# Optimization experiments

Hardware: AMD Instinct MI355X
Metric: run time of the kernel (lower is better)

The kernel has to match this reference:

```python
import jax, jax.numpy as jnp
import numpy as np

N_NODES = 50000
N_EDGES = 1000000
H_DIM = 128
OUT_DIM = 64
N_RELS = 16  # num_bases == num_rels


def setup_inputs() -> dict:
    key = jax.random.key(0)
    ks = jax.random.split(key, 12)
    node_ids = jnp.arange(N_NODES, dtype=jnp.int64) if jax.config.jax_enable_x64 else jnp.arange(N_NODES, dtype=jnp.int32)
    src = jax.random.randint(ks[0], (N_EDGES,), 0, N_NODES)
    dst = jax.random.randint(ks[1], (N_EDGES,), 0, N_NODES)
    etype = jax.random.randint(ks[2], (N_EDGES,), 0, N_RELS)
    norm = jax.random.uniform(ks[3], (N_EDGES, 1), dtype=jnp.float32)
    s1 = 1.0 / np.sqrt(H_DIM)
    s2 = 1.0 / np.sqrt(OUT_DIM)
    emb = jax.random.normal(ks[4], (N_NODES, H_DIM), dtype=jnp.float32)
    V1 = jax.random.normal(ks[5], (N_RELS, H_DIM, H_DIM), dtype=jnp.float32) * s1
    comp1 = jax.random.normal(ks[6], (N_RELS, N_RELS), dtype=jnp.float32) * (1.0 / np.sqrt(N_RELS))
    bias1 = jnp.zeros((H_DIM,), dtype=jnp.float32)
    V2 = jax.random.normal(ks[7], (N_RELS, H_DIM, OUT_DIM), dtype=jnp.float32) * s2
    comp2 = jax.random.normal(ks[8], (N_RELS, N_RELS), dtype=jnp.float32) * (1.0 / np.sqrt(N_RELS))
    bias2 = jnp.zeros((OUT_DIM,), dtype=jnp.float32)
    return {"node_ids": node_ids, "src": src, "dst": dst, "etype": etype, "norm": norm,
            "emb": emb, "V1": V1, "comp1": comp1, "bias1": bias1,
            "V2": V2, "comp2": comp2, "bias2": bias2}


def _rel_graph_conv(x, src, dst, etype, norm, V, comp, bias, num_nodes):
    # Basis decomposition: W_r = sum_b comp[r, b] * V_b  -> [R, in, out]
    W = jnp.einsum('rb,bio->rio', comp, V)
    # Per-relation transform of all nodes: [R, N, out]
    Y = jnp.einsum('ni,rio->rno', x, W)
    # Per-edge message: gather (etype, src) then scale by norm  -> [E, out]
    m = Y[etype, src] * norm
    # Scatter-add to destination nodes
    h = jax.ops.segment_sum(m, dst, num_segments=num_nodes)
    return h + bias


def reference(node_ids, src, dst, etype, norm, emb, V1, comp1, bias1, V2, comp2, bias2):
    x = emb[node_ids]  # [N, H]
    h = jax.nn.relu(_rel_graph_conv(x, src, dst, etype, norm, V1, comp1, bias1, x.shape[0]))
    h = _rel_graph_conv(h, src, dst, etype, norm, V2, comp2, bias2, x.shape[0])
    return h
```

## Files before the change

### kernel.cpp

```cpp
#include <hip/hip_runtime.h>


typedef short bf16x8 __attribute__((ext_vector_type(8)));
typedef float f32x4 __attribute__((ext_vector_type(4)));

#define RELS 16
#define HDIM 128
#define DSTBLK 66
#define MT_P 5
#define CHUNK 32
#define MAXBINS 12288

__device__ inline unsigned short f2bf(float f) {
  unsigned int u = __float_as_uint(f);
  unsigned int r = u + 0x7FFFu + ((u >> 16) & 1u);
  return (unsigned short)(r >> 16);
}

__global__ void cvt_bf16(const float* __restrict__ in, unsigned short* __restrict__ out, int n8) {
  int i = blockIdx.x * blockDim.x + threadIdx.x;
  if (i >= n8) return;
  float4 a = ((const float4*)in)[i * 2];
  float4 b = ((const float4*)in)[i * 2 + 1];
  uint4 o;
  o.x = (unsigned)f2bf(a.x) | ((unsigned)f2bf(a.y) << 16);
  o.y = (unsigned)f2bf(a.z) | ((unsigned)f2bf(a.w) << 16);
  o.z = (unsigned)f2bf(b.x) | ((unsigned)f2bf(b.y) << 16);
  o.w = (unsigned)f2bf(b.z) | ((unsigned)f2bf(b.w) << 16);
  ((uint4*)out)[i] = o;
}

__global__ void compute_w(const float* __restrict__ comp, const float* __restrict__ V,
                          unsigned short* __restrict__ Wt, int IO) {
  int idx = blockIdx.x * blockDim.x + threadIdx.x;
  if (idx >= RELS * IO * HDIM) return;
  int k = idx & (HDIM - 1);
  int o = (idx >> 7) % IO;
  int r = idx / (IO * HDIM);
  float s = 0.f;
#pragma unroll
  for (int b = 0; b < RELS; b++)
    s = fmaf(comp[r * RELS + b], V[(size_t)b * HDIM * IO + (size_t)k * IO + o], s);
  Wt[idx] = f2bf(s);
}

__global__ void hist_bins(const int* __restrict__ dst, const int* __restrict__ etype,
                          int n, int nbins, int* __restrict__ counts) {
  __shared__ int lh[MAXBINS];
  for (int j = threadIdx.x; j < nbins; j += blockDim.x) lh[j] = 0;
  __syncthreads();
  for (int i = blockIdx.x * blockDim.x + threadIdx.x; i < n; i += gridDim.x * blockDim.x)
    atomicAdd(&lh[(dst[i] / DSTBLK) * RELS + etype[i]], 1);
  __syncthreads();
  for (int j = threadIdx.x; j < nbins; j += blockDim.x) {
    int c = lh[j];
    if (c) atomicAdd(&counts[j], c);
  }
}

__global__ void scan_offsets(const int* __restrict__ counts, int* __restrict__ offsets, int nbins) {
  __shared__ int csum[256];
  const int t = threadIdx.x;
  const int CH = (nbins + 255) / 256;
  int lo = t * CH, hi = min(lo + CH, nbins);
  int s = 0;
  for (int i = lo; i < hi; i++) s += (counts[i] + 15) & ~15;
  csum[t] = s;
  __syncthreads();
#pragma unroll
  for (int d = 1; d < 256; d <<= 1) {
    int v = (t >= d) ? csum[t - d] : 0;
    __syncthreads();
    csum[t] += v;
    __syncthreads();
  }
  int run = (t == 0) ? 0 : csum[t - 1];
  for (int i = lo; i < hi; i++) {
    offsets[i] = run;
    run += (counts[i] + 15) & ~15;
  }
  if (lo < nbins && hi == nbins) offsets[nbins] = run;
}

__global__ void scatter_bins(const int* __restrict__ src, const int* __restrict__ dst,
                             const int* __restrict__ etype, const float* __restrict__ norm,
                             int n, const int* __restrict__ offsets, int* __restrict__ cursor,
                             uint2* __restrict__ ebuf) {
  for (int i = blockIdx.x * blockDim.x + threadIdx.x; i < n; i += gridDim.x * blockDim.x) {
    int d = dst[i];
    int blk = d / DSTBLK;
    int b = blk * RELS + etype[i];
    int p = offsets[b] + atomicAdd(&cursor[b], 1);
    ebuf[p] = make_uint2((unsigned)src[i] | ((unsigned)(d - blk * DSTBLK) << 20),
                         __float_as_uint(norm[i]));
  }
}

template <int OUT, bool BF16_RELU_OUT>
__launch_bounds__(256, 3)
__global__ void rgcn_layer(const unsigned short* __restrict__ Xb,
                           const unsigned short* __restrict__ Wt,
                           const uint2* __restrict__ ebuf,
                           const int* __restrict__ offsets, const int* __restrict__ counts,
                           const float* __restrict__ bias, void* __restrict__ Hout,
                           int nNodes) {
  constexpr int NT = OUT / 64;
  __shared__ __align__(16) unsigned short xs[2][CHUNK][136];
  __shared__ __align__(16) unsigned short ys[OUT][40];
  __shared__ __align__(16) unsigned short pmat[2][80][40];

  const int t = threadIdx.x;
  const int w = t >> 6;
  const int lane = t & 63;
  const int quad = lane >> 4;
  const int l16 = lane & 15;
  const int r0 = t >> 4;
  const int k8 = t & 15;
  const bool isHandler = (t & 7) == 0;
  const int myCol = t >> 3;
  const int nodeBase = blockIdx.x * DSTBLK;
  const int binBase = blockIdx.x * RELS;
  const int colBase = w * (OUT / 4);

  for (int i = t; i < 2 * CHUNK * 136 / 8; i += 256) ((uint4*)xs)[i] = make_uint4(0, 0, 0, 0);
  for (int i = t; i < OUT * 40 / 8; i += 256) ((uint4*)ys)[i] = make_uint4(0, 0, 0, 0);
  for (int i = t; i < 2 * 80 * 40 / 8; i += 256) ((uint4*)pmat)[i] = make_uint4(0, 0, 0, 0);

  f32x4 pacc[MT_P][NT] = {};

  int bin = 0, base = 0, binEnd = 0, realEnd = 0;
  for (; bin < RELS; bin++) {
    base = offsets[binBase + bin];
    binEnd = offsets[binBase + bin + 1];
    if (base < binEnd) { realEnd = base + counts[binBase + bin]; break; }
  }

  __syncthreads();

  int pdA = -1, pdB = -1;
  if (bin < RELS) {
    int nR = min(CHUNK, realEnd - base);
    if (r0 < nR) {
      uint2 e = ebuf[base + r0];
      *(uint4*)&xs[0][r0][k8 * 8] = *(const uint4*)(Xb + (size_t)(e.x & 0xFFFFFu) * HDIM + k8 * 8);
    }
    if (16 + r0 < nR) {
      uint2 e = ebuf[base + 16 + r0];
      *(uint4*)&xs[0][16 + r0][k8 * 8] = *(const uint4*)(Xb + (size_t)(e.x & 0xFFFFFu) * HDIM + k8 * 8);
    }
    if (isHandler && myCol < nR) {
      uint2 m = ebuf[base + myCol];
      int dl = (int)(m.x >> 20) & 127;
      pmat[0][dl][myCol] = f2bf(__uint_as_float(m.y));
      pdB = dl;
    }
  }
  __syncthreads();

  int cb = 0;
  int curRel = -1;
  bf16x8 wf[4][NT];

  while (bin < RELS) {
    const int nRows = min(CHUNK, realEnd - base);

    if (bin != curRel) {
      curRel = bin;
      const unsigned short* Wr = Wt + (size_t)bin * OUT * HDIM;
#pragma unroll
      for (int ks = 0; ks < 4; ks++)
#pragma unroll
        for (int nt = 0; nt < NT; nt++)
          wf[ks][nt] = *(const bf16x8*)(Wr + (size_t)(colBase + nt * 16 + l16) * HDIM + ks * 32 + quad * 8);
    }

    int nbin = bin, nbase = base + CHUNK, nbinEnd = binEnd, nrealEnd = realEnd;
    if (nbase >= binEnd) {
      for (nbin = bin + 1; nbin < RELS; nbin++) {
        nbase = offsets[binBase + nbin];
        nbinEnd = offsets[binBase + nbin + 1];
        if (nbase < nbinEnd) { nrealEnd = nbase + counts[binBase + nbin]; break; }
      }
    }
    const bool hasNext = nbin < RELS;
    const int nR = hasNext ? min(CHUNK, nrealEnd - nbase) : 0;

    uint2 e0, e1, em;
    if (hasNext) {
      if (r0 < nR) e0 = ebuf[nbase + r0];
      if (16 + r0 < nR) e1 = ebuf[nbase + 16 + r0];
      if (isHandler && myCol < nR) em = ebuf[nbase + myCol];
    }

#pragma unroll
    for (int mt = 0; mt < 2; mt++) {
      if (mt * 16 < nRows) {
        f32x4 dacc[NT] = {};
#pragma unroll
        for (int ks = 0; ks < 4; ks++) {
          bf16x8 a = *(const bf16x8*)&xs[cb][mt * 16 + l16][ks * 32 + quad * 8];
#pragma unroll
          for (int nt = 0; nt < NT; nt++)
            dacc[nt] = __builtin_amdgcn_mfma_f32_16x16x32_bf16(a, wf[ks][nt], dacc[nt], 0, 0, 0);
        }
#pragma unroll
        for (int nt = 0; nt < NT; nt++) {
          uint2 pk;
          pk.x = (unsigned)f2bf(dacc[nt][0]) | ((unsigned)f2bf(dacc[nt][1]) << 16);
          pk.y = (unsigned)f2bf(dacc[nt][2]) | ((unsigned)f2bf(dacc[nt][3]) << 16);
          *(uint2*)&ys[colBase + nt * 16 + l16][mt * 16 + quad * 4] = pk;
        }
      }
    }

    uint4 g0, g1;
    if (hasNext) {
      if (r0 < nR) g0 = *(const uint4*)(Xb + (size_t)(e0.x & 0xFFFFFu) * HDIM + k8 * 8);
      if (16 + r0 < nR) g1 = *(const uint4*)(Xb + (size_t)(e1.x & 0xFFFFFu) * HDIM + k8 * 8);
    }

    {
      bf16x8 bfv[NT];
#pragma unroll
      for (int nt = 0; nt < NT; nt++)
        bfv[nt] = *(const bf16x8*)&ys[colBase + nt * 16 + l16][quad * 8];
#pragma unroll
      for (int mt = 0; mt < MT_P; mt++) {
        bf16x8 a = *(const bf16x8*)&pmat[cb][mt * 16 + l16][quad * 8];
#pragma unroll
        for (int nt = 0; nt < NT; nt++)
          pacc[mt][nt] = __builtin_amdgcn_mfma_f32_16x16x32_bf16(a, bfv[nt], pacc[mt][nt], 0, 0, 0);
      }
    }

    if (hasNext) {
      if (r0 < nR) *(uint4*)&xs[cb ^ 1][r0][k8 * 8] = g0;
      if (16 + r0 < nR) *(uint4*)&xs[cb ^ 1][16 + r0][k8 * 8] = g1;
      if (isHandler) {
        if (pdA >= 0) pmat[cb ^ 1][pdA][myCol] = 0;
        if (myCol < nR) {
          int dl = (int)(em.x >> 20) & 127;
          pmat[cb ^ 1][dl][myCol] = f2bf(__uint_as_float(em.y));
          pdA = dl;
        } else {
          pdA = -1;
        }
      }
    }
    { int tmp = pdA; pdA = pdB; pdB = tmp; }

    if (hasNext) __syncthreads();

    bin = nbin; base = nbase; binEnd = nbinEnd; realEnd = nrealEnd;
    cb ^= 1;
  }

#pragma unroll
  for (int mt = 0; mt < MT_P; mt++) {
#pragma unroll
    for (int reg = 0; reg < 4; reg++) {
      int ld = mt * 16 + quad * 4 + reg;
      int node = nodeBase + ld;
      if (ld < DSTBLK && node < nNodes) {
#pragma unroll
        for (int nt = 0; nt < NT; nt++) {
          int col = colBase + nt * 16 + l16;
          float v = pacc[mt][nt][reg] + bias[col];
          if constexpr (BF16_RELU_OUT)
            ((unsigned short*)Hout)[(size_t)node * OUT + col] = f2bf(fmaxf(v, 0.f));
          else
            ((float*)Hout)[(size_t)node * OUT + col] = v;
        }
      }
    }
  }
}

extern "C" void kernel_launch(void* const* d_in, const int* in_sizes, int n_in,
                              void* d_out, int out_size, void* d_ws, size_t ws_size,
                              hipStream_t stream) {
  const int*   src   = (const int*)d_in[1];
  const int*   dst   = (const int*)d_in[2];
  const int*   etype = (const int*)d_in[3];
  const float* norm  = (const float*)d_in[4];
  const float* emb   = (const float*)d_in[5];
  const float* V1    = (const float*)d_in[6];
  const float* comp1 = (const float*)d_in[7];
  const float* bias1 = (const float*)d_in[8];
  const float* V2    = (const float*)d_in[9];
  const float* comp2 = (const float*)d_in[10];
  const float* bias2 = (const float*)d_in[11];
  float* out = (float*)d_out;

  const int N = in_sizes[0];
  const int E = in_sizes[1];
  const int H = 128, O = 64;
  const int NB = (N + DSTBLK - 1) / DSTBLK;
  const int NBINS = NB * RELS;
  const int EPAD_MAX = E + NBINS * 16;

  char* ws = (char*)d_ws;
  size_t off = 0;
  auto alloc = [&](size_t bytes) -> void* {
    void* p = ws + off;
    off += (bytes + 255) & ~(size_t)255;
    return p;
  };
  unsigned short* W1t  = (unsigned short*)alloc(sizeof(short) * RELS * H * H);
  unsigned short* W2t  = (unsigned short*)alloc(sizeof(short) * RELS * O * H);
  unsigned short* embh = (unsigned short*)alloc(sizeof(short) * (size_t)N * H);
  unsigned short* h1b  = (unsigned short*)alloc(sizeof(short) * (size_t)N * H);
  uint2* ebuf = (uint2*)alloc(sizeof(uint2) * EPAD_MAX);
  int* counts  = (int*)alloc(sizeof(int) * NBINS);
  int* cursor  = (int*)alloc(sizeof(int) * NBINS);
  int* offsets = (int*)alloc(sizeof(int) * (NBINS + 1));

  hipMemsetAsync(counts, 0, sizeof(int) * NBINS, stream);
  hipMemsetAsync(cursor, 0, sizeof(int) * NBINS, stream);

  cvt_bf16<<<((size_t)N * H / 8 + 255) / 256, 256, 0, stream>>>(emb, embh, N * H / 8);
  compute_w<<<(RELS * H * H + 255) / 256, 256, 0, stream>>>(comp1, V1, W1t, H);
  compute_w<<<(RELS * O * H + 255) / 256, 256, 0, stream>>>(comp2, V2, W2t, O);
  hist_bins<<<256, 256, 0, stream>>>(dst, etype, E, NBINS, counts);
  scan_offsets<<<1, 256, 0, stream>>>(counts, offsets, NBINS);
  scatter_bins<<<1024, 256, 0, stream>>>(src, dst, etype, norm, E, offsets, cursor, ebuf);

  rgcn_layer<128, true><<<NB, 256, 0, stream>>>(embh, W1t, ebuf, offsets, counts, bias1, (void*)h1b, N);
  rgcn_layer<64, false><<<NB, 256, 0, stream>>>(h1b, W2t, ebuf, offsets, counts, bias2, (void*)out, N);
}
```

Measured before the change: 462.0 us.

## Precompute chunk descriptors in LDS and deepen edge/gather prefetch pipeline

Builds a per-block table of chunk descriptors (base, rows, relation) in shared memory up front, replacing the per-iteration scan over bin offsets and counts in global memory. The main loop then runs a three-stage software pipeline: edge records are loaded three chunks ahead and the row gather two chunks ahead, so global-memory latency overlaps more MFMA work. The cost is more live registers, which could lower occupancy under the launch bounds. Chunks are also capped at MAXCH per block, so a block with more chunks than that would silently drop work.

```diff
diff --git a/kernel.cpp b/kernel.cpp
--- a/kernel.cpp
+++ b/kernel.cpp
@@ -10,6 +10,7 @@
 #define MT_P 5
 #define CHUNK 32
 #define MAXBINS 12288
+#define MAXCH 96
 
 __device__ inline unsigned short f2bf(float f) {
   unsigned int u = __float_as_uint(f);
@@ -108,6 +109,8 @@
   __shared__ __align__(16) unsigned short xs[2][CHUNK][136];
   __shared__ __align__(16) unsigned short ys[OUT][40];
   __shared__ __align__(16) unsigned short pmat[2][80][40];
+  __shared__ __align__(16) int4 descS[MAXCH];
+  __shared__ int sBase[16], sCnt[16], sStart[17];
 
   const int t = threadIdx.x;
   const int w = t >> 6;
@@ -126,34 +129,67 @@
   for (int i = t; i < OUT * 40 / 8; i += 256) ((uint4*)ys)[i] = make_uint4(0, 0, 0, 0);
   for (int i = t; i < 2 * 80 * 40 / 8; i += 256) ((uint4*)pmat)[i] = make_uint4(0, 0, 0, 0);
 
+  if (t < 16) {
+    sBase[t] = offsets[binBase + t];
+    sCnt[t] = counts[binBase + t];
+  }
+  __syncthreads();
+  if (t == 0) {
+    int run = 0;
+#pragma unroll
+    for (int b = 0; b < 16; b++) {
+      sStart[b] = run;
+      run += (sCnt[b] + CHUNK - 1) / CHUNK;
+    }
+    sStart[16] = min(run, MAXCH);
+  }
+  __syncthreads();
+  if (t < 16) {
+    int st = sStart[t], ba = sBase[t], c = sCnt[t];
+    for (int j = 0; j * CHUNK < c; j++)
+      if (st + j < MAXCH)
+        descS[st + j] = make_int4(ba + j * CHUNK, min(CHUNK, c - j * CHUNK), t, 0);
+  }
+  __syncthreads();
+  const int nCh = sStart[16];
+
   f32x4 pacc[MT_P][NT] = {};
 
-  int bin = 0, base = 0, binEnd = 0, realEnd = 0;
-  for (; bin < RELS; bin++) {
-    base = offsets[binBase + bin];
-    binEnd = offsets[binBase + bin + 1];
-    if (base < binEnd) { realEnd = base + counts[binBase + bin]; break; }
-  }
-
-  __syncthreads();
-
+  uint2 EnE0, EnE1, EnEm;
+  uint2 En2E0, En2E1, En2Em;
+  uint4 GnG0, GnG1;
+  int n1 = 0, n2 = 0;
   int pdA = -1, pdB = -1;
-  if (bin < RELS) {
-    int nR = min(CHUNK, realEnd - base);
-    if (r0 < nR) {
-      uint2 e = ebuf[base + r0];
-      *(uint4*)&xs[0][r0][k8 * 8] = *(const uint4*)(Xb + (size_t)(e.x & 0xFFFFFu) * HDIM + k8 * 8);
-    }
-    if (16 + r0 < nR) {
-      uint2 e = ebuf[base + 16 + r0];
-      *(uint4*)&xs[0][16 + r0][k8 * 8] = *(const uint4*)(Xb + (size_t)(e.x & 0xFFFFFu) * HDIM + k8 * 8);
-    }
-    if (isHandler && myCol < nR) {
-      uint2 m = ebuf[base + myCol];
-      int dl = (int)(m.x >> 20) & 127;
-      pmat[0][dl][myCol] = f2bf(__uint_as_float(m.y));
+
+  if (nCh > 0) {
+    int4 d0 = descS[0];
+    int4 d1 = (nCh > 1) ? descS[1] : make_int4(0, 0, 0, 0);
+    int4 d2 = (nCh > 2) ? descS[2] : make_int4(0, 0, 0, 0);
+    n1 = d1.y;
+    n2 = d2.y;
+    uint2 a0, a1, am;
+    if (r0 < d0.y) a0 = ebuf[d0.x + r0];
+    if (16 + r0 < d0.y) a1 = ebuf[d0.x + 16 + r0];
+    if (isHandler && myCol < d0.y) am = ebuf[d0.x + myCol];
+    if (r0 < n1) EnE0 = ebuf[d1.x + r0];
+    if (16 + r0 < n1) EnE1 = ebuf[d1.x + 16 + r0];
+    if (isHandler && myCol < n1) EnEm = ebuf[d1.x + myCol];
+    if (r0 < n2) En2E0 = ebuf[d2.x + r0];
+    if (16 + r0 < n2) En2E1 = ebuf[d2.x + 16 + r0];
+    if (isHandler && myCol < n2) En2Em = ebuf[d2.x + myCol];
+    if (r0 < d0.y)
+      *(uint4*)&xs[0][r0][k8 * 8] =
+          *(const uint4*)(Xb + (size_t)(a0.x & 0xFFFFFu) * HDIM + k8 * 8);
+    if (16 + r0 < d0.y)
+      *(uint4*)&xs[0][16 + r0][k8 * 8] =
+          *(const uint4*)(Xb + (size_t)(a1.x & 0xFFFFFu) * HDIM + k8 * 8);
+    if (isHandler && myCol < d0.y) {
+      int dl = (int)(am.x >> 20) & 127;
+      pmat[0][dl][myCol] = f2bf(__uint_as_float(am.y));
       pdB = dl;
     }
+    if (r0 < n1) GnG0 = *(const uint4*)(Xb + (size_t)(EnE0.x & 0xFFFFFu) * HDIM + k8 * 8);
+    if (16 + r0 < n1) GnG1 = *(const uint4*)(Xb + (size_t)(EnE1.x & 0xFFFFFu) * HDIM + k8 * 8);
   }
   __syncthreads();
 
@@ -161,12 +197,13 @@
   int curRel = -1;
   bf16x8 wf[4][NT];
 
-  while (bin < RELS) {
-    const int nRows = min(CHUNK, realEnd - base);
-
-    if (bin != curRel) {
-      curRel = bin;
-      const unsigned short* Wr = Wt + (size_t)bin * OUT * HDIM;
+  for (int ci = 0; ci < nCh; ci++) {
+    int4 dc = descS[ci];
+    const int nRows = dc.y;
+
+    if (dc.z != curRel) {
+      curRel = dc.z;
+      const unsigned short* Wr = Wt + (size_t)curRel * OUT * HDIM;
 #pragma unroll
       for (int ks = 0; ks < 4; ks++)
 #pragma unroll
@@ -174,23 +211,12 @@
           wf[ks][nt] = *(const bf16x8*)(Wr + (size_t)(colBase + nt * 16 + l16) * HDIM + ks * 32 + quad * 8);
     }
 
-    int nbin = bin, nbase = base + CHUNK, nbinEnd = binEnd, nrealEnd = realEnd;
-    if (nbase >= binEnd) {
-      for (nbin = bin + 1; nbin < RELS; nbin++) {
-        nbase = offsets[binBase + nbin];
-        nbinEnd = offsets[binBase + nbin + 1];
-        if (nbase < nbinEnd) { nrealEnd = nbase + counts[binBase + nbin]; break; }
-      }
-    }
-    const bool hasNext = nbin < RELS;
-    const int nR = hasNext ? min(CHUNK, nrealEnd - nbase) : 0;
-
-    uint2 e0, e1, em;
-    if (hasNext) {
-      if (r0 < nR) e0 = ebuf[nbase + r0];
-      if (16 + r0 < nR) e1 = ebuf[nbase + 16 + r0];
-      if (isHandler && myCol < nR) em = ebuf[nbase + myCol];
-    }
+    int4 d3 = make_int4(0, 0, 0, 0);
+    if (ci + 3 < nCh) d3 = descS[ci + 3];
+    uint2 EwE0, EwE1, EwEm;
+    if (r0 < d3.y) EwE0 = ebuf[d3.x + r0];
+    if (16 + r0 < d3.y) EwE1 = ebuf[d3.x + 16 + r0];
+    if (isHandler && myCol < d3.y) EwEm = ebuf[d3.x + myCol];
 
 #pragma unroll
     for (int mt = 0; mt < 2; mt++) {
@@ -213,11 +239,9 @@
       }
     }
 
-    uint4 g0, g1;
-    if (hasNext) {
-      if (r0 < nR) g0 = *(const uint4*)(Xb + (size_t)(e0.x & 0xFFFFFu) * HDIM + k8 * 8);
-      if (16 + r0 < nR) g1 = *(const uint4*)(Xb + (size_t)(e1.x & 0xFFFFFu) * HDIM + k8 * 8);
-    }
+    uint4 GwG0, GwG1;
+    if (r0 < n2) GwG0 = *(const uint4*)(Xb + (size_t)(En2E0.x & 0xFFFFFu) * HDIM + k8 * 8);
+    if (16 + r0 < n2) GwG1 = *(const uint4*)(Xb + (size_t)(En2E1.x & 0xFFFFFu) * HDIM + k8 * 8);
 
     {
       bf16x8 bfv[NT];
@@ -233,25 +257,26 @@
       }
     }
 
-    if (hasNext) {
-      if (r0 < nR) *(uint4*)&xs[cb ^ 1][r0][k8 * 8] = g0;
-      if (16 + r0 < nR) *(uint4*)&xs[cb ^ 1][16 + r0][k8 * 8] = g1;
-      if (isHandler) {
-        if (pdA >= 0) pmat[cb ^ 1][pdA][myCol] = 0;
-        if (myCol < nR) {
-          int dl = (int)(em.x >> 20) & 127;
-          pmat[cb ^ 1][dl][myCol] = f2bf(__uint_as_float(em.y));
-          pdA = dl;
-        } else {
-          pdA = -1;
-        }
+    if (r0 < n1) *(uint4*)&xs[cb ^ 1][r0][k8 * 8] = GnG0;
+    if (16 + r0 < n1) *(uint4*)&xs[cb ^ 1][16 + r0][k8 * 8] = GnG1;
+    if (isHandler) {
+      if (pdA >= 0) pmat[cb ^ 1][pdA][myCol] = 0;
+      if (myCol < n1) {
+        int dl = (int)(EnEm.x >> 20) & 127;
+        pmat[cb ^ 1][dl][myCol] = f2bf(__uint_as_float(EnEm.y));
+        pdA = dl;
+      } else {
+        pdA = -1;
       }
     }
     { int tmp = pdA; pdA = pdB; pdB = tmp; }
 
-    if (hasNext) __syncthreads();
-
-    bin = nbin; base = nbase; binEnd = nbinEnd; realEnd = nrealEnd;
+    EnE0 = En2E0; EnE1 = En2E1; EnEm = En2Em;
+    En2E0 = EwE0; En2E1 = EwE1; En2Em = EwEm;
+    GnG0 = GwG0; GnG1 = GwG1;
+    n1 = n2; n2 = d3.y;
+
+    if (ci + 1 < nCh) __syncthreads();
     cb ^= 1;
   }
 
```

Result: faster. 419.8 us (-9.1%).
